# Kernel tuning notes

Measured on AMD Instinct MI355X. Metric: run time of the kernel, lower is better.

## Reference

```python
import jax, jax.numpy as jnp
import numpy as np

B, S, D, H = 8, 1024, 1024, 16
HD = D // H


def setup_inputs() -> dict:
    key = jax.random.key(0)
    ks = jax.random.split(key, 7)
    sd = 1.0 / np.sqrt(D)
    return {
        "x": jax.random.normal(ks[0], (B, S, D), dtype=jnp.float32),
        "Wq": jax.random.normal(ks[1], (D, D), dtype=jnp.float32) * sd,
        "bq": jnp.zeros((D,), dtype=jnp.float32),
        "Wk": jax.random.normal(ks[2], (D, D), dtype=jnp.float32) * sd,
        "bk": jnp.zeros((D,), dtype=jnp.float32),
        "Wv": jax.random.normal(ks[3], (D, D), dtype=jnp.float32) * sd,
        "bv": jnp.zeros((D,), dtype=jnp.float32),
    }


def reference(x, Wq, bq, Wk, bk, Wv, bv):
    # separate Q/K/V projections (as in the source)
    q = x @ Wq + bq
    k = x @ Wk + bk
    v = x @ Wv + bv
    # [B, H, S, HD]
    q = q.reshape(B, S, H, HD).transpose(0, 2, 1, 3)
    k = k.reshape(B, S, H, HD).transpose(0, 2, 1, 3)
    v = v.reshape(B, S, H, HD).transpose(0, 2, 1, 3)
    scale = jnp.sqrt(jnp.float32(D))  # note: sqrt(embed_dim), faithful to source
    scores = jnp.einsum("bhqd,bhkd->bhqk", q, k) / scale
    attn_prob = jax.nn.softmax(scores, axis=-1)  # [B, H, S, S]
    out = jnp.einsum("bhqk,bhkd->bhqd", attn_prob, v)
    out = out.transpose(0, 2, 1, 3).reshape(B, S, D)
    return out, attn_prob
```

## Files before the change

### kernel.cpp

```cpp
#include <hip/hip_runtime.h>
#include <stdint.h>

#define B_ 8
#define S_ 1024
#define D_ 1024
#define H_ 16
#define HD_ 64
#define KPAD 72
#define PPAD 136

typedef short bf16x8 __attribute__((ext_vector_type(8)));
typedef float f32x4 __attribute__((ext_vector_type(4)));

__device__ __forceinline__ unsigned short f2bf(float f) {
    union { float f; unsigned int u; } v; v.f = f;
    unsigned int r = v.u + 0x7FFFu + ((v.u >> 16) & 1u);
    return (unsigned short)(r >> 16);
}

__global__ __launch_bounds__(256) void cast_x_kernel(const float* __restrict__ x,
                                                     unsigned short* __restrict__ xb, int n4) {
    int i = blockIdx.x * 256 + threadIdx.x;
    if (i >= n4) return;
    float4 v = ((const float4*)x)[i];
    ushort4 o;
    o.x = f2bf(v.x); o.y = f2bf(v.y); o.z = f2bf(v.z); o.w = f2bf(v.w);
    ((ushort4*)xb)[i] = o;
}

__global__ __launch_bounds__(256) void transpose_w_kernel(const float* __restrict__ Wq,
                                                          const float* __restrict__ Wk,
                                                          const float* __restrict__ Wv,
                                                          unsigned short* __restrict__ Wt) {
    __shared__ float t[32][33];
    const int z = blockIdx.z;
    const float* W = (z == 0) ? Wq : (z == 1 ? Wk : Wv);
    int bx = blockIdx.x * 32, by = blockIdx.y * 32;
    int tx = threadIdx.x, ty = threadIdx.y;
    for (int i = 0; i < 4; i++)
        t[ty + 8 * i][tx] = W[(size_t)(by + ty + 8 * i) * D_ + bx + tx];
    __syncthreads();
    unsigned short* o = Wt + (size_t)z * D_ * D_;
    for (int i = 0; i < 4; i++)
        o[(size_t)(bx + ty + 8 * i) * D_ + by + tx] = f2bf(t[tx][ty + 8 * i]);
}

__global__ __launch_bounds__(256) void qkv_gemm_kernel(const unsigned short* __restrict__ Xb,
                                                       const unsigned short* __restrict__ Wt,
                                                       const float* __restrict__ bq,
                                                       const float* __restrict__ bk,
                                                       const float* __restrict__ bv,
                                                       unsigned short* __restrict__ Yb) {
    __shared__ unsigned short Xs[128 * KPAD];
    __shared__ unsigned short Ws[128 * KPAD];

    const int which = blockIdx.y >> 3;
    const int n0 = (blockIdx.y & 7) * 128;
    const int m0 = blockIdx.x * 128;
    const int tid = threadIdx.x;
    const int wave = tid >> 6, lane = tid & 63, quad = lane >> 4, l15 = lane & 15;

    const float* bias = (which == 0) ? bq : (which == 1 ? bk : bv);
    const float scale = (which == 0) ? 0.03125f : 1.0f;
    const unsigned short* Wm = Wt + (size_t)which * D_ * D_;

    f32x4 zero = {0.f, 0.f, 0.f, 0.f};
    f32x4 acc[2][8];
    for (int mt = 0; mt < 2; mt++)
        for (int nt = 0; nt < 8; nt++) acc[mt][nt] = zero;

    for (int kt = 0; kt < 16; kt++) {
        const int k0 = kt * 64;
        __syncthreads();
        for (int i = 0; i < 4; i++) {
            int c = tid + 256 * i;
            int row = c >> 3, cc = (c & 7) * 8;
            *(int4*)&Xs[row * KPAD + cc] = *(const int4*)&Xb[(size_t)(m0 + row) * D_ + k0 + cc];
            *(int4*)&Ws[row * KPAD + cc] = *(const int4*)&Wm[(size_t)(n0 + row) * D_ + k0 + cc];
        }
        __syncthreads();
        bf16x8 af[2][2];
        for (int mt = 0; mt < 2; mt++)
            for (int ks = 0; ks < 2; ks++)
                af[mt][ks] = *(const bf16x8*)&Xs[(wave * 32 + mt * 16 + l15) * KPAD + ks * 32 + quad * 8];
        for (int nt = 0; nt < 8; nt++) {
            bf16x8 b0 = *(const bf16x8*)&Ws[(nt * 16 + l15) * KPAD + quad * 8];
            bf16x8 b1 = *(const bf16x8*)&Ws[(nt * 16 + l15) * KPAD + 32 + quad * 8];
            for (int mt = 0; mt < 2; mt++) {
                acc[mt][nt] = __builtin_amdgcn_mfma_f32_16x16x32_bf16(af[mt][0], b0, acc[mt][nt], 0, 0, 0);
                acc[mt][nt] = __builtin_amdgcn_mfma_f32_16x16x32_bf16(af[mt][1], b1, acc[mt][nt], 0, 0, 0);
            }
        }
    }

    unsigned short* Y = Yb + (size_t)which * (size_t)(B_ * S_) * D_;
    for (int mt = 0; mt < 2; mt++) {
        int rbase = m0 + wave * 32 + mt * 16 + quad * 4;
        for (int nt = 0; nt < 8; nt++) {
            int col = n0 + nt * 16 + l15;
            float bcol = bias[col];
            for (int r = 0; r < 4; r++) {
                float v = (acc[mt][nt][r] + bcol) * scale;
                Y[(size_t)(rbase + r) * D_ + col] = f2bf(v);
            }
        }
    }
}

__global__ __launch_bounds__(256) void attn_kernel(const unsigned short* __restrict__ Qb,
                                                   const unsigned short* __restrict__ Kb,
                                                   const unsigned short* __restrict__ Vb,
                                                   float* __restrict__ out,
                                                   float* __restrict__ attnp) {
    __shared__ unsigned short Ks[128 * KPAD];
    __shared__ unsigned short Vt[64 * PPAD];
    __shared__ unsigned short Ps[128 * PPAD];

    const int bh = blockIdx.y;
    const int b = bh >> 4, h = bh & 15;
    const int q0 = blockIdx.x * 128;
    const int tid = threadIdx.x;
    const int wave = tid >> 6, lane = tid & 63, quad = lane >> 4, l15 = lane & 15;

    bf16x8 qf[2][2];
    for (int mt = 0; mt < 2; mt++)
        for (int ks = 0; ks < 2; ks++)
            qf[mt][ks] = *(const bf16x8*)&Qb[(size_t)(b * S_ + q0 + wave * 32 + mt * 16 + l15) * D_ +
                                            h * HD_ + ks * 32 + quad * 8];

    float mrun[2][4], lrun[2][4];
    for (int mt = 0; mt < 2; mt++)
        for (int r = 0; r < 4; r++) { mrun[mt][r] = -1e30f; lrun[mt][r] = 0.f; }

    f32x4 zero = {0.f, 0.f, 0.f, 0.f};

    for (int kt = 0; kt < 8; kt++) {
        __syncthreads();
        for (int i = 0; i < 4; i++) {
            int c = tid + 256 * i;
            int row = c >> 3, cc = (c & 7) * 8;
            *(int4*)&Ks[row * KPAD + cc] = *(const int4*)&Kb[(size_t)(b * S_ + kt * 128 + row) * D_ + h * HD_ + cc];
        }
        __syncthreads();
        f32x4 acc[2][8];
        for (int mt = 0; mt < 2; mt++)
            for (int nt = 0; nt < 8; nt++) acc[mt][nt] = zero;
        for (int nt = 0; nt < 8; nt++) {
            bf16x8 b0 = *(const bf16x8*)&Ks[(nt * 16 + l15) * KPAD + quad * 8];
            bf16x8 b1 = *(const bf16x8*)&Ks[(nt * 16 + l15) * KPAD + 32 + quad * 8];
            for (int mt = 0; mt < 2; mt++) {
                acc[mt][nt] = __builtin_amdgcn_mfma_f32_16x16x32_bf16(qf[mt][0], b0, acc[mt][nt], 0, 0, 0);
                acc[mt][nt] = __builtin_amdgcn_mfma_f32_16x16x32_bf16(qf[mt][1], b1, acc[mt][nt], 0, 0, 0);
            }
        }
        for (int mt = 0; mt < 2; mt++) {
            for (int r = 0; r < 4; r++) {
                float tm = acc[mt][0][r];
                for (int nt = 1; nt < 8; nt++) tm = fmaxf(tm, acc[mt][nt][r]);
                for (int d = 1; d < 16; d <<= 1) tm = fmaxf(tm, __shfl_xor(tm, d));
                float mnew = fmaxf(mrun[mt][r], tm);
                float s = 0.f;
                for (int nt = 0; nt < 8; nt++) s += __expf(acc[mt][nt][r] - mnew);
                for (int d = 1; d < 16; d <<= 1) s += __shfl_xor(s, d);
                lrun[mt][r] = lrun[mt][r] * __expf(mrun[mt][r] - mnew) + s;
                mrun[mt][r] = mnew;
            }
        }
    }

    float invl[2][4];
    for (int mt = 0; mt < 2; mt++)
        for (int r = 0; r < 4; r++) invl[mt][r] = 1.0f / lrun[mt][r];

    f32x4 oacc[2][4];
    for (int mt = 0; mt < 2; mt++)
        for (int nv = 0; nv < 4; nv++) oacc[mt][nv] = zero;

    float* attn_base = attnp + (size_t)bh * S_ * S_;

    for (int kt = 0; kt < 8; kt++) {
        __syncthreads();
        for (int i = 0; i < 4; i++) {
            int c = tid + 256 * i;
            int row = c >> 3, cc = (c & 7) * 8;
            *(int4*)&Ks[row * KPAD + cc] = *(const int4*)&Kb[(size_t)(b * S_ + kt * 128 + row) * D_ + h * HD_ + cc];
            union { int4 v; unsigned short u[8]; } uu;
            uu.v = *(const int4*)&Vb[(size_t)(b * S_ + kt * 128 + row) * D_ + h * HD_ + cc];
            for (int j = 0; j < 8; j++) Vt[(cc + j) * PPAD + row] = uu.u[j];
        }
        __syncthreads();
        f32x4 acc[2][8];
        for (int mt = 0; mt < 2; mt++)
            for (int nt = 0; nt < 8; nt++) acc[mt][nt] = zero;
        for (int nt = 0; nt < 8; nt++) {
            bf16x8 b0 = *(const bf16x8*)&Ks[(nt * 16 + l15) * KPAD + quad * 8];
            bf16x8 b1 = *(const bf16x8*)&Ks[(nt * 16 + l15) * KPAD + 32 + quad * 8];
            for (int mt = 0; mt < 2; mt++) {
                acc[mt][nt] = __builtin_amdgcn_mfma_f32_16x16x32_bf16(qf[mt][0], b0, acc[mt][nt], 0, 0, 0);
                acc[mt][nt] = __builtin_amdgcn_mfma_f32_16x16x32_bf16(qf[mt][1], b1, acc[mt][nt], 0, 0, 0);
            }
        }
        for (int mt = 0; mt < 2; mt++) {
            int rl = wave * 32 + mt * 16 + quad * 4;
            for (int nt = 0; nt < 8; nt++) {
                int cl = nt * 16 + l15;
                for (int r = 0; r < 4; r++) {
                    float p = __expf(acc[mt][nt][r] - mrun[mt][r]) * invl[mt][r];
                    attn_base[(size_t)(q0 + rl + r) * S_ + kt * 128 + cl] = p;
                    Ps[(rl + r) * PPAD + cl] = f2bf(p);
                }
            }
        }
        __syncthreads();
        for (int kc = 0; kc < 4; kc++) {
            bf16x8 af[2];
            for (int mt = 0; mt < 2; mt++)
                af[mt] = *(const bf16x8*)&Ps[(wave * 32 + mt * 16 + l15) * PPAD + kc * 32 + quad * 8];
            for (int nv = 0; nv < 4; nv++) {
                bf16x8 bf = *(const bf16x8*)&Vt[(nv * 16 + l15) * PPAD + kc * 32 + quad * 8];
                for (int mt = 0; mt < 2; mt++)
                    oacc[mt][nv] = __builtin_amdgcn_mfma_f32_16x16x32_bf16(af[mt], bf, oacc[mt][nv], 0, 0, 0);
            }
        }
    }

    for (int mt = 0; mt < 2; mt++) {
        int rbase = q0 + wave * 32 + mt * 16 + quad * 4;
        for (int nv = 0; nv < 4; nv++) {
            int col = h * HD_ + nv * 16 + l15;
            for (int r = 0; r < 4; r++)
                out[(size_t)(b * S_ + rbase + r) * D_ + col] = oacc[mt][nv][r];
        }
    }
}

extern "C" void kernel_launch(void* const* d_in, const int* in_sizes, int n_in,
                              void* d_out, int out_size, void* d_ws, size_t ws_size,
                              hipStream_t stream) {
    const float* x  = (const float*)d_in[0];
    const float* Wq = (const float*)d_in[1];
    const float* bq = (const float*)d_in[2];
    const float* Wk = (const float*)d_in[3];
    const float* bk = (const float*)d_in[4];
    const float* Wv = (const float*)d_in[5];
    const float* bv = (const float*)d_in[6];
    float* out = (float*)d_out;
    float* attnp = out + (size_t)B_ * S_ * D_;

    unsigned short* Xb = (unsigned short*)d_ws;
    unsigned short* Wt = Xb + (size_t)B_ * S_ * D_;
    unsigned short* Yb = Wt + (size_t)3 * D_ * D_;
    unsigned short* Qb = Yb;
    unsigned short* Kb = Yb + (size_t)B_ * S_ * D_;
    unsigned short* Vb = Kb + (size_t)B_ * S_ * D_;

    int n4 = B_ * S_ * D_ / 4;
    cast_x_kernel<<<(n4 + 255) / 256, 256, 0, stream>>>(x, Xb, n4);
    transpose_w_kernel<<<dim3(32, 32, 3), dim3(32, 8), 0, stream>>>(Wq, Wk, Wv, Wt);
    qkv_gemm_kernel<<<dim3(64, 24), 256, 0, stream>>>(Xb, Wt, bq, bk, bv, Yb);
    attn_kernel<<<dim3(8, 128), 256, 0, stream>>>(Qb, Kb, Vb, out, attnp);
}
```

Measured before the change: 814.4 us.

## Vectorize epilogue stores via lane transpose and pre-transpose V in GEMM

Adds a 4x4 in-register transpose across lanes using xor shuffles, so the QKV GEMM, attention probability, and output epilogues can emit float4/ushort4 stores instead of scalar strided ones. The QKV GEMM now writes V already transposed per head, which replaces the scalar LDS scatter transpose in the attention kernel with vector loads. The GEMM wave tiling also changes from 32x128 to 64x64 per wave, which improves fragment reuse. The cost is extra shuffles and a strided-column global write pattern for V in the GEMM epilogue.

```diff
diff --git a/kernel.cpp b/kernel.cpp
--- a/kernel.cpp
+++ b/kernel.cpp
@@ -7,6 +7,7 @@
 #define H_ 16
 #define HD_ 64
 #define KPAD 72
+#define VPAD 136
 #define PPAD 136
 
 typedef short bf16x8 __attribute__((ext_vector_type(8)));
@@ -16,6 +17,20 @@
     union { float f; unsigned int u; } v; v.f = f;
     unsigned int r = v.u + 0x7FFFu + ((v.u >> 16) & 1u);
     return (unsigned short)(r >> 16);
+}
+
+__device__ __forceinline__ void xpose4(float v[4]) {
+    const int ln = threadIdx.x & 3;
+    float x0 = (ln & 1) ? v[0] : v[1];
+    float x1 = (ln & 1) ? v[2] : v[3];
+    x0 = __shfl_xor(x0, 1);
+    x1 = __shfl_xor(x1, 1);
+    if (ln & 1) { v[0] = x0; v[2] = x1; } else { v[1] = x0; v[3] = x1; }
+    float y0 = (ln & 2) ? v[0] : v[2];
+    float y1 = (ln & 2) ? v[1] : v[3];
+    y0 = __shfl_xor(y0, 2);
+    y1 = __shfl_xor(y1, 2);
+    if (ln & 2) { v[0] = y0; v[1] = y1; } else { v[2] = y0; v[3] = y1; }
 }
 
 __global__ __launch_bounds__(256) void cast_x_kernel(const float* __restrict__ x,
@@ -59,15 +74,16 @@
     const int m0 = blockIdx.x * 128;
     const int tid = threadIdx.x;
     const int wave = tid >> 6, lane = tid & 63, quad = lane >> 4, l15 = lane & 15;
+    const int wm = wave >> 1, wn = wave & 1;
 
     const float* bias = (which == 0) ? bq : (which == 1 ? bk : bv);
     const float scale = (which == 0) ? 0.03125f : 1.0f;
     const unsigned short* Wm = Wt + (size_t)which * D_ * D_;
 
     f32x4 zero = {0.f, 0.f, 0.f, 0.f};
-    f32x4 acc[2][8];
-    for (int mt = 0; mt < 2; mt++)
-        for (int nt = 0; nt < 8; nt++) acc[mt][nt] = zero;
+    f32x4 acc[4][4];
+    for (int mt = 0; mt < 4; mt++)
+        for (int nt = 0; nt < 4; nt++) acc[mt][nt] = zero;
 
     for (int kt = 0; kt < 16; kt++) {
         const int k0 = kt * 64;
@@ -79,29 +95,51 @@
             *(int4*)&Ws[row * KPAD + cc] = *(const int4*)&Wm[(size_t)(n0 + row) * D_ + k0 + cc];
         }
         __syncthreads();
-        bf16x8 af[2][2];
-        for (int mt = 0; mt < 2; mt++)
+        bf16x8 af[4][2];
+        for (int mt = 0; mt < 4; mt++)
             for (int ks = 0; ks < 2; ks++)
-                af[mt][ks] = *(const bf16x8*)&Xs[(wave * 32 + mt * 16 + l15) * KPAD + ks * 32 + quad * 8];
-        for (int nt = 0; nt < 8; nt++) {
-            bf16x8 b0 = *(const bf16x8*)&Ws[(nt * 16 + l15) * KPAD + quad * 8];
-            bf16x8 b1 = *(const bf16x8*)&Ws[(nt * 16 + l15) * KPAD + 32 + quad * 8];
-            for (int mt = 0; mt < 2; mt++) {
+                af[mt][ks] = *(const bf16x8*)&Xs[(wm * 64 + mt * 16 + l15) * KPAD + ks * 32 + quad * 8];
+        for (int nt = 0; nt < 4; nt++) {
+            bf16x8 b0 = *(const bf16x8*)&Ws[(wn * 64 + nt * 16 + l15) * KPAD + quad * 8];
+            bf16x8 b1 = *(const bf16x8*)&Ws[(wn * 64 + nt * 16 + l15) * KPAD + 32 + quad * 8];
+            for (int mt = 0; mt < 4; mt++) {
                 acc[mt][nt] = __builtin_amdgcn_mfma_f32_16x16x32_bf16(af[mt][0], b0, acc[mt][nt], 0, 0, 0);
                 acc[mt][nt] = __builtin_amdgcn_mfma_f32_16x16x32_bf16(af[mt][1], b1, acc[mt][nt], 0, 0, 0);
             }
         }
     }
 
-    unsigned short* Y = Yb + (size_t)which * (size_t)(B_ * S_) * D_;
-    for (int mt = 0; mt < 2; mt++) {
-        int rbase = m0 + wave * 32 + mt * 16 + quad * 4;
-        for (int nt = 0; nt < 8; nt++) {
-            int col = n0 + nt * 16 + l15;
-            float bcol = bias[col];
-            for (int r = 0; r < 4; r++) {
-                float v = (acc[mt][nt][r] + bcol) * scale;
-                Y[(size_t)(rbase + r) * D_ + col] = f2bf(v);
+    if (which < 2) {
+        unsigned short* Y = Yb + (size_t)which * (size_t)(B_ * S_) * D_;
+        for (int mt = 0; mt < 4; mt++) {
+            int rbase = m0 + wm * 64 + mt * 16 + quad * 4;
+            for (int nt = 0; nt < 4; nt++) {
+                int colL = n0 + wn * 64 + nt * 16 + l15;
+                float bcol = bias[colL];
+                float p[4];
+                for (int r = 0; r < 4; r++) p[r] = (acc[mt][nt][r] + bcol) * scale;
+                xpose4(p);
+                int row = rbase + (l15 & 3);
+                int col = n0 + wn * 64 + nt * 16 + (l15 >> 2) * 4;
+                ushort4 o;
+                o.x = f2bf(p[0]); o.y = f2bf(p[1]); o.z = f2bf(p[2]); o.w = f2bf(p[3]);
+                *(ushort4*)&Y[(size_t)row * D_ + col] = o;
+            }
+        }
+    } else {
+        unsigned short* Vt = Yb + (size_t)2 * (size_t)(B_ * S_) * D_;
+        for (int mt = 0; mt < 4; mt++) {
+            int m = m0 + wm * 64 + mt * 16 + quad * 4;
+            int bb = m >> 10, s = m & 1023;
+            for (int nt = 0; nt < 4; nt++) {
+                int col = n0 + wn * 64 + nt * 16 + l15;
+                float bcol = bias[col];
+                ushort4 o;
+                o.x = f2bf(acc[mt][nt][0] + bcol);
+                o.y = f2bf(acc[mt][nt][1] + bcol);
+                o.z = f2bf(acc[mt][nt][2] + bcol);
+                o.w = f2bf(acc[mt][nt][3] + bcol);
+                *(ushort4*)&Vt[((size_t)(bb * 16 + (col >> 6)) * 64 + (col & 63)) * S_ + s] = o;
             }
         }
     }
@@ -109,11 +147,11 @@
 
 __global__ __launch_bounds__(256) void attn_kernel(const unsigned short* __restrict__ Qb,
                                                    const unsigned short* __restrict__ Kb,
-                                                   const unsigned short* __restrict__ Vb,
+                                                   const unsigned short* __restrict__ Vtg,
                                                    float* __restrict__ out,
                                                    float* __restrict__ attnp) {
     __shared__ unsigned short Ks[128 * KPAD];
-    __shared__ unsigned short Vt[64 * PPAD];
+    __shared__ unsigned short Vts[64 * VPAD];
     __shared__ unsigned short Ps[128 * PPAD];
 
     const int bh = blockIdx.y;
@@ -121,6 +159,8 @@
     const int q0 = blockIdx.x * 128;
     const int tid = threadIdx.x;
     const int wave = tid >> 6, lane = tid & 63, quad = lane >> 4, l15 = lane & 15;
+
+    const unsigned short* Vg = Vtg + (size_t)(b * 16 + h) * 64 * S_;
 
     bf16x8 qf[2][2];
     for (int mt = 0; mt < 2; mt++)
@@ -182,11 +222,10 @@
         __syncthreads();
         for (int i = 0; i < 4; i++) {
             int c = tid + 256 * i;
-            int row = c >> 3, cc = (c & 7) * 8;
-            *(int4*)&Ks[row * KPAD + cc] = *(const int4*)&Kb[(size_t)(b * S_ + kt * 128 + row) * D_ + h * HD_ + cc];
-            union { int4 v; unsigned short u[8]; } uu;
-            uu.v = *(const int4*)&Vb[(size_t)(b * S_ + kt * 128 + row) * D_ + h * HD_ + cc];
-            for (int j = 0; j < 8; j++) Vt[(cc + j) * PPAD + row] = uu.u[j];
+            int krow = c >> 3, kcc = (c & 7) * 8;
+            *(int4*)&Ks[krow * KPAD + kcc] = *(const int4*)&Kb[(size_t)(b * S_ + kt * 128 + krow) * D_ + h * HD_ + kcc];
+            int vrow = c >> 4, vcc = (c & 15) * 8;
+            *(int4*)&Vts[vrow * VPAD + vcc] = *(const int4*)&Vg[(size_t)vrow * S_ + kt * 128 + vcc];
         }
         __syncthreads();
         f32x4 acc[2][8];
@@ -201,14 +240,18 @@
             }
         }
         for (int mt = 0; mt < 2; mt++) {
-            int rl = wave * 32 + mt * 16 + quad * 4;
             for (int nt = 0; nt < 8; nt++) {
-                int cl = nt * 16 + l15;
-                for (int r = 0; r < 4; r++) {
-                    float p = __expf(acc[mt][nt][r] - mrun[mt][r]) * invl[mt][r];
-                    attn_base[(size_t)(q0 + rl + r) * S_ + kt * 128 + cl] = p;
-                    Ps[(rl + r) * PPAD + cl] = f2bf(p);
-                }
+                float p[4];
+                for (int r = 0; r < 4; r++)
+                    p[r] = __expf(acc[mt][nt][r] - mrun[mt][r]) * invl[mt][r];
+                xpose4(p);
+                int rl = wave * 32 + mt * 16 + quad * 4 + (l15 & 3);
+                int cl = nt * 16 + (l15 >> 2) * 4;
+                float4 f4; f4.x = p[0]; f4.y = p[1]; f4.z = p[2]; f4.w = p[3];
+                *(float4*)&attn_base[(size_t)(q0 + rl) * S_ + kt * 128 + cl] = f4;
+                unsigned int lo = ((unsigned int)f2bf(p[1]) << 16) | f2bf(p[0]);
+                unsigned int hi = ((unsigned int)f2bf(p[3]) << 16) | f2bf(p[2]);
+                *(uint2*)&Ps[rl * PPAD + cl] = make_uint2(lo, hi);
             }
         }
         __syncthreads();
@@ -217,19 +260,22 @@
             for (int mt = 0; mt < 2; mt++)
                 af[mt] = *(const bf16x8*)&Ps[(wave * 32 + mt * 16 + l15) * PPAD + kc * 32 + quad * 8];
             for (int nv = 0; nv < 4; nv++) {
-                bf16x8 bf = *(const bf16x8*)&Vt[(nv * 16 + l15) * PPAD + kc * 32 + quad * 8];
+                bf16x8 bfv = *(const bf16x8*)&Vts[(nv * 16 + l15) * VPAD + kc * 32 + quad * 8];
                 for (int mt = 0; mt < 2; mt++)
-                    oacc[mt][nv] = __builtin_amdgcn_mfma_f32_16x16x32_bf16(af[mt], bf, oacc[mt][nv], 0, 0, 0);
+                    oacc[mt][nv] = __builtin_amdgcn_mfma_f32_16x16x32_bf16(af[mt], bfv, oacc[mt][nv], 0, 0, 0);
             }
         }
     }
 
     for (int mt = 0; mt < 2; mt++) {
-        int rbase = q0 + wave * 32 + mt * 16 + quad * 4;
         for (int nv = 0; nv < 4; nv++) {
-            int col = h * HD_ + nv * 16 + l15;
-            for (int r = 0; r < 4; r++)
-                out[(size_t)(b * S_ + rbase + r) * D_ + col] = oacc[mt][nv][r];
+            float o[4];
+            for (int r = 0; r < 4; r++) o[r] = oacc[mt][nv][r];
+            xpose4(o);
+            int row = q0 + wave * 32 + mt * 16 + quad * 4 + (l15 & 3);
+            int col = h * HD_ + nv * 16 + (l15 >> 2) * 4;
+            float4 f4; f4.x = o[0]; f4.y = o[1]; f4.z = o[2]; f4.w = o[3];
+            *(float4*)&out[(size_t)(b * S_ + row) * D_ + col] = f4;
         }
     }
 }
@@ -252,11 +298,11 @@
     unsigned short* Yb = Wt + (size_t)3 * D_ * D_;
     unsigned short* Qb = Yb;
     unsigned short* Kb = Yb + (size_t)B_ * S_ * D_;
-    unsigned short* Vb = Kb + (size_t)B_ * S_ * D_;
+    unsigned short* Vtg = Kb + (size_t)B_ * S_ * D_;
 
     int n4 = B_ * S_ * D_ / 4;
     cast_x_kernel<<<(n4 + 255) / 256, 256, 0, stream>>>(x, Xb, n4);
     transpose_w_kernel<<<dim3(32, 32, 3), dim3(32, 8), 0, stream>>>(Wq, Wk, Wv, Wt);
     qkv_gemm_kernel<<<dim3(64, 24), 256, 0, stream>>>(Xb, Wt, bq, bk, bv, Yb);
-    attn_kernel<<<dim3(8, 128), 256, 0, stream>>>(Qb, Kb, Vb, out, attnp);
-}
+    attn_kernel<<<dim3(8, 128), 256, 0, stream>>>(Qb, Kb, Vtg, out, attnp);
+}
```

After: 837.7 us. +2.9%, slower.
